# Optimization experiments

Measured on AMD Instinct MI355X. Metric: run time of the kernel, lower is better.

The kernel has to match this reference:

```python
import math
import jax, jax.numpy as jnp
import numpy as np

HEADS = 8


def setup_inputs() -> dict:
    key = jax.random.key(0)
    k1, k2 = jax.random.split(key)
    b, heads, c, t, s_enc = 4, HEADS, 64, 1024, 1024
    x = jax.random.normal(k1, (b, 3 * heads * c, t), dtype=jnp.float32)
    encoder_kv = jax.random.normal(k2, (b, 2 * heads * c, s_enc), dtype=jnp.float32)
    return {"x": x, "encoder_kv": encoder_kv}


def reference(x, encoder_kv):
    heads = HEADS
    b, ch3, t = x.shape
    c = ch3 // (3 * heads)
    s_enc = encoder_kv.shape[-1]
    # 'b (qkv heads c) h -> qkv (b heads) c h'
    qkv = x.reshape(b, 3, heads, c, t).transpose(1, 0, 2, 3, 4).reshape(3, b * heads, c, t)
    q, k, v = qkv[0], qkv[1], qkv[2]
    ekv = encoder_kv.reshape(b, 2, heads, c, s_enc).transpose(1, 0, 2, 3, 4).reshape(2, b * heads, c, s_enc)
    ek, ev = ekv[0], ekv[1]
    k = jnp.concatenate([ek, k], axis=-1)  # (bh, c, s_enc + t)
    v = jnp.concatenate([ev, v], axis=-1)
    scale = 1.0 / math.sqrt(math.sqrt(c))
    weight = jnp.einsum('bct,bcs->bts', q * scale, k * scale)  # (bh, t, s)
    weight = jax.nn.softmax(weight.astype(jnp.float32), axis=-1).astype(weight.dtype)
    out = jnp.einsum('bts,bcs->bct', weight, v)  # (bh, c, t)
    # '(b heads) c h -> b (heads c) h'
    out = out.reshape(b, heads, c, t).reshape(b, heads * c, t)
    return out
```

## Files before the change

kernel.cpp:

```cpp
#include <hip/hip_runtime.h>

typedef __attribute__((ext_vector_type(8))) short bf16x8;
typedef __attribute__((ext_vector_type(16))) float f32x16;
typedef __attribute__((ext_vector_type(4))) float f32x4;
typedef __attribute__((ext_vector_type(4))) unsigned int u32x4;

#define NH 8
#define CD 64
#define TLEN 1024
#define SENC 1024
#define STOT 2048
#define NGRP 4
#define KRANGE (STOT / NGRP)
#define SKG 32
#define NITG (KRANGE / SKG)
#define BQ 64
#define QSCALE 0.18033688f

#define KFS 2048
#define VFS 2048

__device__ __forceinline__ ushort f2bf(float f) {
  uint x = __builtin_bit_cast(uint, f);
  uint r = (x + 0x7fffu + ((x >> 16) & 1u)) >> 16;
  return (ushort)r;
}
__device__ __forceinline__ uint4 pack8(const ushort* p) {
  uint4 u;
  u.x = (uint)p[0] | ((uint)p[1] << 16);
  u.y = (uint)p[2] | ((uint)p[3] << 16);
  u.z = (uint)p[4] | ((uint)p[5] << 16);
  u.w = (uint)p[6] | ((uint)p[7] << 16);
  return u;
}
__device__ __forceinline__ uint cvtpk(float lo, float hi) {
  uint r;
  asm("v_cvt_pk_bf16_f32 %0, %1, %2" : "=v"(r) : "v"(lo), "v"(hi));
  return r;
}
__device__ __forceinline__ void plswap(uint& a, uint& b) {
  asm("v_permlane32_swap_b32 %0, %1" : "+v"(a), "+v"(b));
}
__device__ __forceinline__ bf16x8 mk8(uint a, uint b, uint c, uint d) {
  u32x4 t = {a, b, c, d};
  return __builtin_bit_cast(bf16x8, t);
}

__global__ __launch_bounds__(256)
void repack_kernel(const float* __restrict__ x, const float* __restrict__ ekv,
                   ushort* __restrict__ ktf, ushort* __restrict__ vtf) {
  const int kx = blockIdx.x;
  const int bh = blockIdx.y;
  const int b = bh >> 3, h = bh & 7;
  const int t = threadIdx.x;
  const float* ks;
  const float* vs;
  if (kx < 16) {
    ks = ekv + (size_t)(b * 2 * NH * CD + h * CD) * SENC + kx * 64;
    vs = ekv + (size_t)(b * 2 * NH * CD + NH * CD + h * CD) * SENC + kx * 64;
  } else {
    ks = x + (size_t)(b * 3 * NH * CD + NH * CD + h * CD) * TLEN + (kx - 16) * 64;
    vs = x + (size_t)(b * 3 * NH * CD + 2 * NH * CD + h * CD) * TLEN + (kx - 16) * 64;
  }
  if (blockIdx.z == 0) {
    __shared__ float Lt[64 * 65];
    const int ci = t >> 2, seg = t & 3;
#pragma unroll
    for (int j = 0; j < 4; ++j) {
      float4 d = *(const float4*)&ks[ci * 1024 + seg * 16 + 4 * j];
      Lt[ci * 65 + seg * 16 + 4 * j + 0] = d.x;
      Lt[ci * 65 + seg * 16 + 4 * j + 1] = d.y;
      Lt[ci * 65 + seg * 16 + 4 * j + 2] = d.z;
      Lt[ci * 65 + seg * 16 + 4 * j + 3] = d.w;
    }
    __syncthreads();
    const int key = t >> 2;
    ushort tmp[16];
#pragma unroll
    for (int u = 0; u < 16; ++u)
      tmp[u] = f2bf(Lt[(seg * 16 + u) * 65 + key]);
    const int kt2 = kx * 2 + (key >> 5);
    const int al = key & 31;
    ushort* d0 = ktf + ((((size_t)bh * 64 + kt2) * 4 + seg) * 64 + 0 * 32 + al) * 8;
    ushort* d1 = ktf + ((((size_t)bh * 64 + kt2) * 4 + seg) * 64 + 1 * 32 + al) * 8;
    *(uint4*)d0 = pack8(tmp);
    *(uint4*)d1 = pack8(tmp + 8);
  } else {
    const int ci = t >> 2, seg = t & 3;
    ushort tmp[16];
#pragma unroll
    for (int j = 0; j < 4; ++j) {
      float4 d = *(const float4*)&vs[ci * 1024 + seg * 16 + 4 * j];
      tmp[4 * j + 0] = f2bf(d.x);
      tmp[4 * j + 1] = f2bf(d.y);
      tmp[4 * j + 2] = f2bf(d.z);
      tmp[4 * j + 3] = f2bf(d.w);
    }
    const int kt2 = kx * 2 + (seg >> 1);
    const int s = seg & 1;
    const int mtc = ci >> 5;
    const int al = ci & 31;
    ushort* d0 = vtf + (((((size_t)bh * 64 + kt2) * 2 + s) * 2 + mtc) * 64 + 0 * 32 + al) * 8;
    ushort* d1 = vtf + (((((size_t)bh * 64 + kt2) * 2 + s) * 2 + mtc) * 64 + 1 * 32 + al) * 8;
    *(uint4*)d0 = pack8(tmp);
    *(uint4*)d1 = pack8(tmp + 8);
  }
}

__global__ __launch_bounds__(512, 4)
void qkv_attn_ws(const float* __restrict__ x, const ushort* __restrict__ ktf,
                 const ushort* __restrict__ vtf, float* __restrict__ out) {
  __shared__ float fa[8960];

  const int tid  = threadIdx.x;
  const int w    = tid >> 6;
  const int qcol = w & 1;
  const int grp  = w >> 1;
  const int lane = tid & 63;
  const int al   = lane & 31;
  const int h    = lane >> 5;

  const int f  = blockIdx.x;
  const int bh = (f & 7) | (((f >> 7) & 3) << 3);
  const int qt = (f >> 3) & 15;
  const int b  = bh >> 3;
  const int hh = bh & 7;
  const int t0 = qt * BQ;

  const float* qg = x + (size_t)(b * 3 * NH * CD + hh * CD) * TLEN;
  float* og = out + (size_t)(b * NH * CD + hh * CD) * TLEN;

  const ushort* kfb = ktf + ((size_t)bh * 64 + grp * 16) * KFS + (size_t)lane * 8;
  const ushort* vfb = vtf + ((size_t)bh * 64 + grp * 16) * VFS + (size_t)lane * 8;

  const int q_l = qcol * 32 + al;
  const float* qp = qg + t0 + q_l;
  float qv[4][8];
#pragma unroll
  for (int kst = 0; kst < 4; ++kst)
#pragma unroll
    for (int j = 0; j < 8; ++j)
      qv[kst][j] = qp[(size_t)(kst * 16 + h * 8 + j) * TLEN] * QSCALE;
  bf16x8 qfrag[4];
#pragma unroll
  for (int kst = 0; kst < 4; ++kst)
    qfrag[kst] = mk8(cvtpk(qv[kst][0], qv[kst][1]), cvtpk(qv[kst][2], qv[kst][3]),
                     cvtpk(qv[kst][4], qv[kst][5]), cvtpk(qv[kst][6], qv[kst][7]));

  f32x16 of0, of1;
#pragma unroll
  for (int i = 0; i < 16; ++i) { of0[i] = 0.f; of1[i] = 0.f; }
  float l_acc = 0.f;

#pragma unroll 2
  for (int it = 0; it < NITG; ++it) {
    const ushort* kp = kfb + (size_t)it * KFS;
    const ushort* vp = vfb + (size_t)it * VFS;
    bf16x8 kf0 = *(const bf16x8*)(kp + 0 * 512);
    bf16x8 kf1 = *(const bf16x8*)(kp + 1 * 512);
    bf16x8 kf2 = *(const bf16x8*)(kp + 2 * 512);
    bf16x8 kf3 = *(const bf16x8*)(kp + 3 * 512);
    bf16x8 va0 = *(const bf16x8*)(vp + 0 * 512);
    bf16x8 vb0 = *(const bf16x8*)(vp + 1 * 512);
    bf16x8 va1 = *(const bf16x8*)(vp + 2 * 512);
    bf16x8 vb1 = *(const bf16x8*)(vp + 3 * 512);

    f32x16 acc;
#pragma unroll
    for (int i = 0; i < 16; ++i) acc[i] = 0.f;
    acc = __builtin_amdgcn_mfma_f32_32x32x16_bf16(kf0, qfrag[0], acc, 0, 0, 0);
    acc = __builtin_amdgcn_mfma_f32_32x32x16_bf16(kf1, qfrag[1], acc, 0, 0, 0);
    acc = __builtin_amdgcn_mfma_f32_32x32x16_bf16(kf2, qfrag[2], acc, 0, 0, 0);
    acc = __builtin_amdgcn_mfma_f32_32x32x16_bf16(kf3, qfrag[3], acc, 0, 0, 0);

    uint ulo[4], uhi[4];
#pragma unroll
    for (int rq = 0; rq < 4; ++rq) {
      float p0 = exp2f(acc[4 * rq + 0]);
      float p1 = exp2f(acc[4 * rq + 1]);
      float p2 = exp2f(acc[4 * rq + 2]);
      float p3 = exp2f(acc[4 * rq + 3]);
      l_acc += (p0 + p1) + (p2 + p3);
      ulo[rq] = cvtpk(p0, p1);
      uhi[rq] = cvtpk(p2, p3);
    }

    bf16x8 pfr[2];
#pragma unroll
    for (int kst = 0; kst < 2; ++kst) {
      uint xlo = ulo[2 * kst], ylo = ulo[2 * kst + 1];
      uint xhi = uhi[2 * kst], yhi = uhi[2 * kst + 1];
      plswap(xlo, ylo);
      plswap(xhi, yhi);
      pfr[kst] = mk8(xlo, xhi, ylo, yhi);
    }

    of0 = __builtin_amdgcn_mfma_f32_32x32x16_bf16(va0, pfr[0], of0, 0, 0, 0);
    of0 = __builtin_amdgcn_mfma_f32_32x32x16_bf16(va1, pfr[1], of0, 0, 0, 0);
    of1 = __builtin_amdgcn_mfma_f32_32x32x16_bf16(vb0, pfr[0], of1, 0, 0, 0);
    of1 = __builtin_amdgcn_mfma_f32_32x32x16_bf16(vb1, pfr[1], of1, 0, 0, 0);
  }

  __syncthreads();
  float* tA = fa;
  float* tB = fa + 64 * 68;
  float* lf = fa + 2 * 64 * 68;
  float lv = l_acc + __shfl_xor(l_acc, 32);
  if (h == 0) lf[grp * 64 + q_l] = lv;

  if (grp >= 2) {
    float* T = (grp == 2) ? tA : tB;
#pragma unroll
    for (int rq = 0; rq < 4; ++rq) {
      *(f32x4*)&T[q_l * 68 + 8 * rq + 4 * h] =
          f32x4{of0[4 * rq + 0], of0[4 * rq + 1], of0[4 * rq + 2], of0[4 * rq + 3]};
      *(f32x4*)&T[q_l * 68 + 32 + 8 * rq + 4 * h] =
          f32x4{of1[4 * rq + 0], of1[4 * rq + 1], of1[4 * rq + 2], of1[4 * rq + 3]};
    }
  }
  __syncthreads();
  if (grp < 2) {
    const float* T = (grp == 0) ? tA : tB;
#pragma unroll
    for (int rq = 0; rq < 4; ++rq) {
      f32x4 a = *(const f32x4*)&T[q_l * 68 + 8 * rq + 4 * h];
      f32x4 c = *(const f32x4*)&T[q_l * 68 + 32 + 8 * rq + 4 * h];
#pragma unroll
      for (int j = 0; j < 4; ++j) { of0[4 * rq + j] += a[j]; of1[4 * rq + j] += c[j]; }
    }
  }
  __syncthreads();
  if (grp == 1) {
#pragma unroll
    for (int rq = 0; rq < 4; ++rq) {
      *(f32x4*)&tA[q_l * 68 + 8 * rq + 4 * h] =
          f32x4{of0[4 * rq + 0], of0[4 * rq + 1], of0[4 * rq + 2], of0[4 * rq + 3]};
      *(f32x4*)&tA[q_l * 68 + 32 + 8 * rq + 4 * h] =
          f32x4{of1[4 * rq + 0], of1[4 * rq + 1], of1[4 * rq + 2], of1[4 * rq + 3]};
    }
  }
  __syncthreads();
  if (grp == 0) {
#pragma unroll
    for (int rq = 0; rq < 4; ++rq) {
      f32x4 a = *(const f32x4*)&tA[q_l * 68 + 8 * rq + 4 * h];
      f32x4 c = *(const f32x4*)&tA[q_l * 68 + 32 + 8 * rq + 4 * h];
#pragma unroll
      for (int j = 0; j < 4; ++j) { of0[4 * rq + j] += a[j]; of1[4 * rq + j] += c[j]; }
    }
    float lsum = lf[q_l] + lf[64 + q_l] + lf[128 + q_l] + lf[192 + q_l];
    float inv = 1.0f / lsum;
    float* ob = og + t0 + q_l;
#pragma unroll
    for (int r = 0; r < 16; ++r) {
      int ci = (r & 3) + 8 * (r >> 2) + 4 * h;
      ob[(size_t)ci * TLEN] = of0[r] * inv;
      ob[(size_t)(32 + ci) * TLEN] = of1[r] * inv;
    }
  }
}

extern "C" void kernel_launch(void* const* d_in, const int* in_sizes, int n_in,
                              void* d_out, int out_size, void* d_ws, size_t ws_size,
                              hipStream_t stream) {
  const float* x   = (const float*)d_in[0];
  const float* ekv = (const float*)d_in[1];
  float* out = (float*)d_out;
  ushort* ktf = (ushort*)d_ws;
  ushort* vtf = ktf + (size_t)32 * 64 * KFS;
  repack_kernel<<<dim3(32, 32, 2), 256, 0, stream>>>(x, ekv, ktf, vtf);
  qkv_attn_ws<<<32 * 16, 512, 0, stream>>>(x, ktf, vtf, out);
}
```

Measured before the change: 118.0 us.

## Split key range across eight wave groups with 32-query blocks

Each block now covers 32 queries instead of 64, and its 8 waves each take one-eighth of the key range instead of splitting into 2 query columns by 4 key groups. The grid doubles to 1024 blocks and the launch-bounds occupancy hint rises to 8, to raise parallelism and occupancy across CUs. The cost is a deeper cross-wave reduction through shared memory (three rounds of barriers) and each K/V fragment being reused by half as many queries per block, which increases K/V traffic.

```diff
diff --git a/kernel.cpp b/kernel.cpp
--- a/kernel.cpp
+++ b/kernel.cpp
@@ -10,11 +10,11 @@
 #define TLEN 1024
 #define SENC 1024
 #define STOT 2048
-#define NGRP 4
+#define NGRP 8
 #define KRANGE (STOT / NGRP)
 #define SKG 32
 #define NITG (KRANGE / SKG)
-#define BQ 64
+#define BQ 32
 #define QSCALE 0.18033688f
 
 #define KFS 2048
@@ -107,22 +107,20 @@
   }
 }
 
-__global__ __launch_bounds__(512, 4)
+__global__ __launch_bounds__(512, 8)
 void qkv_attn_ws(const float* __restrict__ x, const ushort* __restrict__ ktf,
                  const ushort* __restrict__ vtf, float* __restrict__ out) {
   __shared__ float fa[8960];
 
   const int tid  = threadIdx.x;
-  const int w    = tid >> 6;
-  const int qcol = w & 1;
-  const int grp  = w >> 1;
+  const int grp  = tid >> 6;
   const int lane = tid & 63;
   const int al   = lane & 31;
   const int h    = lane >> 5;
 
   const int f  = blockIdx.x;
-  const int bh = (f & 7) | (((f >> 7) & 3) << 3);
-  const int qt = (f >> 3) & 15;
+  const int bh = (f & 7) | (((f >> 8) & 3) << 3);
+  const int qt = (f >> 3) & 31;
   const int b  = bh >> 3;
   const int hh = bh & 7;
   const int t0 = qt * BQ;
@@ -130,10 +128,10 @@
   const float* qg = x + (size_t)(b * 3 * NH * CD + hh * CD) * TLEN;
   float* og = out + (size_t)(b * NH * CD + hh * CD) * TLEN;
 
-  const ushort* kfb = ktf + ((size_t)bh * 64 + grp * 16) * KFS + (size_t)lane * 8;
-  const ushort* vfb = vtf + ((size_t)bh * 64 + grp * 16) * VFS + (size_t)lane * 8;
-
-  const int q_l = qcol * 32 + al;
+  const ushort* kfb = ktf + ((size_t)bh * 64 + grp * 8) * KFS + (size_t)lane * 8;
+  const ushort* vfb = vtf + ((size_t)bh * 64 + grp * 8) * VFS + (size_t)lane * 8;
+
+  const int q_l = al;
   const float* qp = qg + t0 + q_l;
   float qv[4][8];
 #pragma unroll
@@ -202,53 +200,50 @@
   }
 
   __syncthreads();
-  float* tA = fa;
-  float* tB = fa + 64 * 68;
-  float* lf = fa + 2 * 64 * 68;
+  float* lf = fa + 8704;
   float lv = l_acc + __shfl_xor(l_acc, 32);
-  if (h == 0) lf[grp * 64 + q_l] = lv;
-
-  if (grp >= 2) {
-    float* T = (grp == 2) ? tA : tB;
-#pragma unroll
-    for (int rq = 0; rq < 4; ++rq) {
-      *(f32x4*)&T[q_l * 68 + 8 * rq + 4 * h] =
-          f32x4{of0[4 * rq + 0], of0[4 * rq + 1], of0[4 * rq + 2], of0[4 * rq + 3]};
-      *(f32x4*)&T[q_l * 68 + 32 + 8 * rq + 4 * h] =
-          f32x4{of1[4 * rq + 0], of1[4 * rq + 1], of1[4 * rq + 2], of1[4 * rq + 3]};
-    }
-  }
-  __syncthreads();
-  if (grp < 2) {
-    const float* T = (grp == 0) ? tA : tB;
-#pragma unroll
-    for (int rq = 0; rq < 4; ++rq) {
-      f32x4 a = *(const f32x4*)&T[q_l * 68 + 8 * rq + 4 * h];
-      f32x4 c = *(const f32x4*)&T[q_l * 68 + 32 + 8 * rq + 4 * h];
-#pragma unroll
-      for (int j = 0; j < 4; ++j) { of0[4 * rq + j] += a[j]; of1[4 * rq + j] += c[j]; }
-    }
-  }
-  __syncthreads();
-  if (grp == 1) {
-#pragma unroll
-    for (int rq = 0; rq < 4; ++rq) {
-      *(f32x4*)&tA[q_l * 68 + 8 * rq + 4 * h] =
-          f32x4{of0[4 * rq + 0], of0[4 * rq + 1], of0[4 * rq + 2], of0[4 * rq + 3]};
-      *(f32x4*)&tA[q_l * 68 + 32 + 8 * rq + 4 * h] =
-          f32x4{of1[4 * rq + 0], of1[4 * rq + 1], of1[4 * rq + 2], of1[4 * rq + 3]};
-    }
-  }
+  if (h == 0) lf[grp * 32 + q_l] = lv;
+
+#define OF_WRITE(T)                                                          \
+  {                                                                          \
+    float* Tp = (T);                                                         \
+    _Pragma("unroll") for (int rq = 0; rq < 4; ++rq) {                       \
+      *(f32x4*)&Tp[q_l * 68 + 8 * rq + 4 * h] =                              \
+          f32x4{of0[4 * rq + 0], of0[4 * rq + 1], of0[4 * rq + 2],           \
+                of0[4 * rq + 3]};                                            \
+      *(f32x4*)&Tp[q_l * 68 + 32 + 8 * rq + 4 * h] =                         \
+          f32x4{of1[4 * rq + 0], of1[4 * rq + 1], of1[4 * rq + 2],           \
+                of1[4 * rq + 3]};                                            \
+    }                                                                        \
+  }
+#define OF_ADD(T)                                                            \
+  {                                                                          \
+    const float* Tp = (T);                                                   \
+    _Pragma("unroll") for (int rq = 0; rq < 4; ++rq) {                       \
+      f32x4 a = *(const f32x4*)&Tp[q_l * 68 + 8 * rq + 4 * h];               \
+      f32x4 c = *(const f32x4*)&Tp[q_l * 68 + 32 + 8 * rq + 4 * h];          \
+      _Pragma("unroll") for (int j = 0; j < 4; ++j) {                        \
+        of0[4 * rq + j] += a[j];                                             \
+        of1[4 * rq + j] += c[j];                                             \
+      }                                                                      \
+    }                                                                        \
+  }
+
+  if (grp >= 4) OF_WRITE(fa + (grp - 4) * 2176);
+  __syncthreads();
+  if (grp < 4) OF_ADD(fa + grp * 2176);
+  __syncthreads();
+  if (grp == 2 || grp == 3) OF_WRITE(fa + (grp - 2) * 2176);
+  __syncthreads();
+  if (grp < 2) OF_ADD(fa + grp * 2176);
+  __syncthreads();
+  if (grp == 1) OF_WRITE(fa);
   __syncthreads();
   if (grp == 0) {
-#pragma unroll
-    for (int rq = 0; rq < 4; ++rq) {
-      f32x4 a = *(const f32x4*)&tA[q_l * 68 + 8 * rq + 4 * h];
-      f32x4 c = *(const f32x4*)&tA[q_l * 68 + 32 + 8 * rq + 4 * h];
-#pragma unroll
-      for (int j = 0; j < 4; ++j) { of0[4 * rq + j] += a[j]; of1[4 * rq + j] += c[j]; }
-    }
-    float lsum = lf[q_l] + lf[64 + q_l] + lf[128 + q_l] + lf[192 + q_l];
+    OF_ADD(fa);
+    float lsum = 0.f;
+#pragma unroll
+    for (int g = 0; g < 8; ++g) lsum += lf[g * 32 + q_l];
     float inv = 1.0f / lsum;
     float* ob = og + t0 + q_l;
 #pragma unroll
@@ -258,6 +253,8 @@
       ob[(size_t)(32 + ci) * TLEN] = of1[r] * inv;
     }
   }
+#undef OF_WRITE
+#undef OF_ADD
 }
 
 extern "C" void kernel_launch(void* const* d_in, const int* in_sizes, int n_in,
@@ -269,5 +266,5 @@
   ushort* ktf = (ushort*)d_ws;
   ushort* vtf = ktf + (size_t)32 * 64 * KFS;
   repack_kernel<<<dim3(32, 32, 2), 256, 0, stream>>>(x, ekv, ktf, vtf);
-  qkv_attn_ws<<<32 * 16, 512, 0, stream>>>(x, ktf, vtf, out);
-}
+  qkv_attn_ws<<<32 * 32, 512, 0, stream>>>(x, ktf, vtf, out);
+}
```

After: 279.1 us. 136% more time.
